# Kernel tuning notes

Measured on AMD Instinct MI355X. Metric: run time of the kernel, lower is better.

Reference implementation:

```python
import jax, jax.numpy as jnp
import numpy as np

N, E, DIN, DOUT, H = 50000, 800000, 256, 128, 8
DH = DOUT // H  # per-head dim = 16


def setup_inputs() -> dict:
    key = jax.random.key(0)
    k1, k2, k3, k4, k5 = jax.random.split(key, 5)
    x = jax.random.normal(k1, (N, DIN), dtype=jnp.float32)
    edge_index = jax.random.randint(k2, (2, E), 0, N)
    W_trans = jax.random.normal(k3, (DOUT, DIN), dtype=jnp.float32) / np.sqrt(DIN).astype(np.float32)
    W_att = jax.random.normal(k4, (1, 2 * DH), dtype=jnp.float32) / np.sqrt(2 * DH).astype(np.float32)
    b_att = jax.random.normal(k5, (1,), dtype=jnp.float32) * 0.01
    return {"x": x, "W_trans": W_trans, "W_att": W_att, "b_att": b_att, "edge_index": edge_index}


def reference(x, W_trans, W_att, b_att, edge_index):
    n = x.shape[0]
    # append self-loops (as in the torch module)
    loops = jnp.arange(n, dtype=edge_index.dtype)
    ei = jnp.concatenate([edge_index, jnp.stack([loops, loops])], axis=1)  # [2, E+N]
    src, dst = ei[0], ei[1]

    # linear transform, split heads: [n, H, DH]
    h = (x @ W_trans.T).reshape(n, H, DH)
    h_i = h[src]  # [Etot, H, DH]
    h_j = h[dst]  # [Etot, H, DH]

    # per-edge attention score: concat -> linear -> leaky_relu(0.2)
    s = jnp.concatenate([h_i, h_j], axis=-1) @ W_att.T + b_att  # [Etot, H, 1]
    s = jnp.where(s >= 0, s, 0.2 * s)

    # softmax(dim=0)*exp_sum/scatter_add(exp) == exp(s)/segment_sum(exp(s)) per dst node
    e = jnp.exp(s)
    denom = jax.ops.segment_sum(e, dst, num_segments=n)  # [n, H, 1]
    att = e / denom[dst]

    out = jax.ops.segment_sum(h_i * att, dst, num_segments=n)  # [n, H, DH]
    return out.reshape(n, DOUT)  # head_fusion='cat'
```

## Files before the change

### kernel.cpp

```cpp
#include <hip/hip_runtime.h>


constexpr int DIN  = 256;
constexpr int DOUT = 128;
constexpr int H    = 8;
constexpr int CAP  = 5120;
constexpr int NRANGE = 5;
constexpr int CHUNK = 4096;

typedef __attribute__((ext_vector_type(8))) short bf16x8;
typedef __attribute__((ext_vector_type(4))) float f32x4;

__device__ __forceinline__ float lrelu(float s) { return s >= 0.0f ? s : 0.2f * s; }

__device__ __forceinline__ unsigned short f2bf(float f) {
  unsigned u = __float_as_uint(f);
  u += 0x7FFF + ((u >> 16) & 1);
  return (unsigned short)(u >> 16);
}
__device__ __forceinline__ float bflo(unsigned u) { return __uint_as_float(u << 16); }
__device__ __forceinline__ float bfhi(unsigned u) { return __uint_as_float(u & 0xFFFF0000u); }
__device__ __forceinline__ int rng5(int s) {
  return (int)__umulhi((unsigned)s, 429497u);
}

__device__ __forceinline__ int wave_incl_scan(int v, int lane) {
#pragma unroll
  for (int d = 1; d < 64; d <<= 1) {
    int t = __shfl_up(v, d, 64);
    if (lane >= d) v += t;
  }
  return v;
}

__global__ void conv_w(const float* __restrict__ W, unsigned short* __restrict__ Wbf,
                       int n, int* __restrict__ bcount, int nb) {
  int i = blockIdx.x * blockDim.x + threadIdx.x;
  if (i < n) Wbf[i] = f2bf(W[i]);
  if (blockIdx.x == 0 && threadIdx.x < nb) bcount[threadIdx.x] = 0;
}

__global__ __launch_bounds__(256) void bp_gemm(const float* __restrict__ x,
                                               const unsigned short* __restrict__ Wbf,
                                               unsigned short* __restrict__ hbf, int N,
                                               const int* __restrict__ ei,
                                               int* __restrict__ bcount,
                                               unsigned* __restrict__ pair_buf,
                                               int E, int nb, int bp_blocks) {
  __shared__ int hist[256];
  __shared__ int gbase[256];
  if ((int)blockIdx.x < bp_blocks) {
    int c0 = blockIdx.x * CHUNK;
    hist[threadIdx.x] = 0;
    __syncthreads();
    int dcache[16];
#pragma unroll
    for (int q = 0; q < 16; ++q) {
      int e = c0 + q * 256 + threadIdx.x;
      dcache[q] = (e < E) ? ei[E + e] : -1;
      if (dcache[q] >= 0) atomicAdd(&hist[dcache[q] >> 8], 1);
    }
    __syncthreads();
    if (threadIdx.x < nb) {
      int c = hist[threadIdx.x];
      gbase[threadIdx.x] = c ? atomicAdd(&bcount[threadIdx.x], c) : 0;
    }
    __syncthreads();
    hist[threadIdx.x] = 0;
    __syncthreads();
#pragma unroll
    for (int q = 0; q < 16; ++q) {
      int e = c0 + q * 256 + threadIdx.x;
      if (dcache[q] >= 0) {
        int s = ei[e];
        int bk = dcache[q] >> 8;
        int r = atomicAdd(&hist[bk], 1);
        pair_buf[bk * CAP + gbase[bk] + r] = ((unsigned)s << 8) | (unsigned)(dcache[q] & 255);
      }
    }
    return;
  }
  int gb = blockIdx.x - bp_blocks;
  int tid = threadIdx.x;
  int w = tid >> 6, lane = tid & 63;
  int mr = lane & 15, kg = lane >> 4;
  int m0 = gb * 32 + (w >> 1) * 16;
  int nt0 = (w & 1) * 4;
  if (m0 >= N) return;
  int rr = m0 + mr;
  if (rr >= N) rr = N - 1;
  const float* xrow = x + (size_t)rr * DIN + kg * 8;

  float4 xa[8], xc[8];
#pragma unroll
  for (int ks = 0; ks < 8; ++ks) {
    xa[ks] = *(const float4*)(xrow + ks * 32);
    xc[ks] = *(const float4*)(xrow + ks * 32 + 4);
  }

  f32x4 acc[4];
#pragma unroll
  for (int t = 0; t < 4; ++t) acc[t] = (f32x4){0.f, 0.f, 0.f, 0.f};

#pragma unroll
  for (int ks = 0; ks < 8; ++ks) {
    bf16x8 a;
    a[0] = (short)f2bf(xa[ks].x); a[1] = (short)f2bf(xa[ks].y);
    a[2] = (short)f2bf(xa[ks].z); a[3] = (short)f2bf(xa[ks].w);
    a[4] = (short)f2bf(xc[ks].x); a[5] = (short)f2bf(xc[ks].y);
    a[6] = (short)f2bf(xc[ks].z); a[7] = (short)f2bf(xc[ks].w);
#pragma unroll
    for (int t = 0; t < 4; ++t) {
      bf16x8 b = *(const bf16x8*)(Wbf + ((nt0 + t) * 16 + mr) * DIN + ks * 32 + kg * 8);
      acc[t] = __builtin_amdgcn_mfma_f32_16x16x32_bf16(a, b, acc[t], 0, 0, 0);
    }
  }
#pragma unroll
  for (int t = 0; t < 4; ++t) {
#pragma unroll
    for (int r = 0; r < 4; ++r) {
      int row = m0 + kg * 4 + r;
      if (row < N) hbf[row * DOUT + (nt0 + t) * 16 + mr] = f2bf(acc[t][r]);
    }
  }
}

__global__ __launch_bounds__(256) void fs_ns(const unsigned* __restrict__ pair_buf,
                                             const int* __restrict__ bcount,
                                             int* __restrict__ offsets,
                                             uint4* __restrict__ len8,
                                             unsigned short* __restrict__ src_sorted,
                                             const unsigned short* __restrict__ hbf,
                                             const float* __restrict__ Wa,
                                             float* __restrict__ a_src,
                                             float* __restrict__ a_dst,
                                             int N, int E, int nb, int fs_blocks) {
  __shared__ int cnt[128 * NRANGE];
  __shared__ int cur[128 * NRANGE];
  __shared__ int redS[256];
  __shared__ int wsumS[4];
  __shared__ int lowerE;
  const int t = threadIdx.x;
  if ((int)blockIdx.x >= fs_blocks) {
    int idx = ((int)blockIdx.x - fs_blocks) * 256 + t;
    if (idx >= N * H) return;
    int v = idx >> 3, hh = idx & 7;
    const unsigned short* hp = hbf + (size_t)v * DOUT + hh * 16;
    uint4 p0 = *(const uint4*)hp;
    uint4 p1 = *(const uint4*)(hp + 8);
    float hv[16];
    hv[0] = bflo(p0.x); hv[1] = bfhi(p0.x); hv[2] = bflo(p0.y); hv[3] = bfhi(p0.y);
    hv[4] = bflo(p0.z); hv[5] = bfhi(p0.z); hv[6] = bflo(p0.w); hv[7] = bfhi(p0.w);
    hv[8] = bflo(p1.x); hv[9] = bfhi(p1.x); hv[10] = bflo(p1.y); hv[11] = bfhi(p1.y);
    hv[12] = bflo(p1.z); hv[13] = bfhi(p1.z); hv[14] = bflo(p1.w); hv[15] = bfhi(p1.w);
    float s1 = 0.f, s2 = 0.f;
#pragma unroll
    for (int d = 0; d < 16; ++d) {
      s1 += hv[d] * Wa[d];
      s2 += hv[d] * Wa[16 + d];
    }
    a_src[idx] = s1;
    a_dst[idx] = s2;
    return;
  }
  const int b = blockIdx.x;
  const int B = b >> 1, half = b & 1;
  const int node0 = b * 128;
  if (node0 >= N) return;
  for (int i = t; i < 128 * NRANGE; i += 256) cnt[i] = 0;
  if (t == 0) lowerE = 0;
  __syncthreads();
  const int v = node0 + t;
  int r_self = -1;
  if (t < 128 && v < N) {
    r_self = rng5(v);
    cnt[t * NRANGE + r_self] = 1;
  }
  __syncthreads();
  const int cntE = bcount[B];
  const unsigned* reg = pair_buf + B * CAP;
  for (int i = t; i < cntE; i += 256) {
    unsigned p = reg[i];
    int dl = p & 255;
    if ((dl >> 7) == half) atomicAdd(&cnt[(dl & 127) * NRANGE + rng5((int)(p >> 8))], 1);
    else if (half == 1) atomicAdd(&lowerE, 1);
  }
  redS[t] = (t < B) ? bcount[t] : 0;
  __syncthreads();
  for (int s = 128; s > 0; s >>= 1) {
    if (t < s) redS[t] += redS[t + s];
    __syncthreads();
  }
  int csr_base = redS[0] + B * 256 + (half ? (128 + lowerE) : 0);
  int tot = 0;
  if (t < 128) {
#pragma unroll
    for (int r = 0; r < NRANGE; ++r) tot += cnt[t * NRANGE + r];
  }
  int lane = t & 63, wv = t >> 6;
  int inc = wave_incl_scan(tot, lane);
  if (lane == 63) wsumS[wv] = inc;
  __syncthreads();
  int base = 0;
  for (int q = 0; q < wv; ++q) base += wsumS[q];
  int ex = base + inc - tot;
  if (t < 128 && v < N) {
    offsets[v] = csr_base + ex;
    int run = ex, rs_self = 0, c[NRANGE];
#pragma unroll
    for (int r = 0; r < NRANGE; ++r) {
      c[r] = cnt[t * NRANGE + r];
      if (r == r_self) rs_self = run;
      cur[t * NRANGE + r] = run + (r == r_self ? 1 : 0);
      run += c[r];
    }
    src_sorted[csr_base + rs_self] = (unsigned short)v;
    uint4 L;
    L.x = (unsigned)c[0] | ((unsigned)c[1] << 16);
    L.y = (unsigned)c[2] | ((unsigned)c[3] << 16);
    L.z = (unsigned)c[4];
    L.w = 0;
    len8[v] = L;
  }
  if (b == 0 && t == 0) offsets[N] = E + N;
  __syncthreads();
  for (int i = t; i < cntE; i += 256) {
    unsigned p = reg[i];
    int dl = p & 255;
    if ((dl >> 7) == half) {
      int s = (int)(p >> 8);
      int k = atomicAdd(&cur[(dl & 127) * NRANGE + rng5(s)], 1);
      src_sorted[csr_base + k] = (unsigned short)s;
    }
  }
}

__global__ __launch_bounds__(256) void aggregate(const unsigned short* __restrict__ hbf,
                                                 const float* __restrict__ a_src,
                                                 const float* __restrict__ a_dst,
                                                 const float* __restrict__ b_att,
                                                 const int* __restrict__ offsets,
                                                 const uint4* __restrict__ len8,
                                                 const unsigned short* __restrict__ src_sorted,
                                                 float* __restrict__ out, int N) {
  int wid = blockIdx.x * 4 + (threadIdx.x >> 6);
  if (wid >= N) return;
  int lane = threadIdx.x & 63;
  int g = lane >> 4, sl = lane & 15;
  int head = sl >> 1;
  float adv = a_dst[wid * H + head] + b_att[0];
  int j = offsets[wid];
  uint4 L = len8[wid];
  int lens[NRANGE];
  lens[0] = L.x & 0xffff; lens[1] = L.x >> 16;
  lens[2] = L.y & 0xffff; lens[3] = L.y >> 16;
  lens[4] = L.z;
  float a0 = 0, a1 = 0, a2 = 0, a3 = 0, a4 = 0, a5 = 0, a6 = 0, a7 = 0, den = 0;
  for (int r = 0; r < NRANGE; ++r) {
    int end = j + lens[r];
    for (int j0 = j; j0 < end; j0 += 4) {
      int jj = j0 + g;
      bool val = jj < end;
      int jc = val ? jj : end - 1;
      int s = src_sorted[jc];
      float as = a_src[s * H + head];
      uint4 u = *(const uint4*)(hbf + s * DOUT + sl * 8);
      float e = val ? __expf(lrelu(as + adv)) : 0.f;
      den += e;
      a0 += e * bflo(u.x); a1 += e * bfhi(u.x);
      a2 += e * bflo(u.y); a3 += e * bfhi(u.y);
      a4 += e * bflo(u.z); a5 += e * bfhi(u.z);
      a6 += e * bflo(u.w); a7 += e * bfhi(u.w);
    }
    j = end;
  }
  den += __shfl_xor(den, 16, 64); den += __shfl_xor(den, 32, 64);
  a0 += __shfl_xor(a0, 16, 64); a0 += __shfl_xor(a0, 32, 64);
  a1 += __shfl_xor(a1, 16, 64); a1 += __shfl_xor(a1, 32, 64);
  a2 += __shfl_xor(a2, 16, 64); a2 += __shfl_xor(a2, 32, 64);
  a3 += __shfl_xor(a3, 16, 64); a3 += __shfl_xor(a3, 32, 64);
  a4 += __shfl_xor(a4, 16, 64); a4 += __shfl_xor(a4, 32, 64);
  a5 += __shfl_xor(a5, 16, 64); a5 += __shfl_xor(a5, 32, 64);
  a6 += __shfl_xor(a6, 16, 64); a6 += __shfl_xor(a6, 32, 64);
  a7 += __shfl_xor(a7, 16, 64); a7 += __shfl_xor(a7, 32, 64);
  float inv = 1.0f / den;
  if (g == 0) {
    float4 o = make_float4(a0 * inv, a1 * inv, a2 * inv, a3 * inv);
    *(float4*)&out[wid * DOUT + sl * 8] = o;
  } else if (g == 1) {
    float4 o = make_float4(a4 * inv, a5 * inv, a6 * inv, a7 * inv);
    *(float4*)&out[wid * DOUT + sl * 8 + 4] = o;
  }
}

extern "C" void kernel_launch(void* const* d_in, const int* in_sizes, int n_in,
                              void* d_out, int out_size, void* d_ws, size_t ws_size,
                              hipStream_t stream) {
  const float* x     = (const float*)d_in[0];
  const float* W     = (const float*)d_in[1];
  const float* Wa    = (const float*)d_in[2];
  const float* b_att = (const float*)d_in[3];
  const int*   ei    = (const int*)d_in[4];
  const int N  = in_sizes[0] / DIN;
  const int E  = in_sizes[4] / 2;
  const int NB = (N + 255) / 256;
  float* out = (float*)d_out;

  char* p = (char*)d_ws;
  auto take = [&p](size_t bytes) {
    uintptr_t u = ((uintptr_t)p + 15) & ~(uintptr_t)15;
    p = (char*)(u + bytes);
    return (void*)u;
  };
  unsigned short* hbf = (unsigned short*)take((size_t)N * DOUT * 2);
  unsigned short* Wbf = (unsigned short*)take((size_t)DOUT * DIN * 2);
  float* a_src        = (float*)take((size_t)N * H * 4);
  float* a_dst        = (float*)take((size_t)N * H * 4);
  int* bcount         = (int*)take((size_t)NB * 4);
  unsigned* pair_buf  = (unsigned*)take((size_t)NB * CAP * 4);
  int* offsets        = (int*)take((size_t)(N + 1) * 4);
  uint4* len8         = (uint4*)take((size_t)N * 16);
  unsigned short* src_sorted = (unsigned short*)take((size_t)(E + N + 16) * 2);

  dim3 b256(256);
  const int bp_blocks   = (E + CHUNK - 1) / CHUNK;
  const int gemm_blocks = (N + 31) / 32;
  const int fs_blocks   = (N + 127) / 128;
  const int ns_blocks   = (N * H + 255) / 256;

  conv_w<<<dim3((DOUT * DIN + 255) / 256), b256, 0, stream>>>(W, Wbf, DOUT * DIN, bcount, NB);
  bp_gemm<<<dim3(bp_blocks + gemm_blocks), b256, 0, stream>>>(
      x, Wbf, hbf, N, ei, bcount, pair_buf, E, NB, bp_blocks);
  fs_ns<<<dim3(fs_blocks + ns_blocks), b256, 0, stream>>>(
      pair_buf, bcount, offsets, len8, src_sorted, hbf, Wa, a_src, a_dst, N, E, NB, fs_blocks);
  aggregate<<<dim3((N + 3) / 4), b256, 0, stream>>>(hbf, a_src, a_dst, b_att, offsets,
                                                    len8, src_sorted, out, N);
}
```

Measured before the change: 195.4 us.

## Drop source-range sub-bucketing in CSR build and shrink edge-binning chunk size

Removes the per-destination split of neighbors into five source-index ranges (and the len8 side array), so the CSR build uses one counter per node with 256-node blocks instead of two half-blocks. The aggregate kernel now loops over one contiguous neighbor range from offsets. The binning chunk shrinks from 4096 to 1024 edges per block, giving more blocks. The trade-off is simpler sorting and fewer loop boundaries in aggregation, but neighbors are no longer grouped by source range, which the old layout presumably used for gather cache locality.

```diff
diff --git a/kernel.cpp b/kernel.cpp
--- a/kernel.cpp
+++ b/kernel.cpp
@@ -5,8 +5,7 @@
 constexpr int DOUT = 128;
 constexpr int H    = 8;
 constexpr int CAP  = 5120;
-constexpr int NRANGE = 5;
-constexpr int CHUNK = 4096;
+constexpr int CHUNK = 1024;
 
 typedef __attribute__((ext_vector_type(8))) short bf16x8;
 typedef __attribute__((ext_vector_type(4))) float f32x4;
@@ -20,9 +19,6 @@
 }
 __device__ __forceinline__ float bflo(unsigned u) { return __uint_as_float(u << 16); }
 __device__ __forceinline__ float bfhi(unsigned u) { return __uint_as_float(u & 0xFFFF0000u); }
-__device__ __forceinline__ int rng5(int s) {
-  return (int)__umulhi((unsigned)s, 429497u);
-}
 
 __device__ __forceinline__ int wave_incl_scan(int v, int lane) {
 #pragma unroll
@@ -53,9 +49,9 @@
     int c0 = blockIdx.x * CHUNK;
     hist[threadIdx.x] = 0;
     __syncthreads();
-    int dcache[16];
-#pragma unroll
-    for (int q = 0; q < 16; ++q) {
+    int dcache[4];
+#pragma unroll
+    for (int q = 0; q < 4; ++q) {
       int e = c0 + q * 256 + threadIdx.x;
       dcache[q] = (e < E) ? ei[E + e] : -1;
       if (dcache[q] >= 0) atomicAdd(&hist[dcache[q] >> 8], 1);
@@ -69,7 +65,7 @@
     hist[threadIdx.x] = 0;
     __syncthreads();
 #pragma unroll
-    for (int q = 0; q < 16; ++q) {
+    for (int q = 0; q < 4; ++q) {
       int e = c0 + q * 256 + threadIdx.x;
       if (dcache[q] >= 0) {
         int s = ei[e];
@@ -128,21 +124,19 @@
 __global__ __launch_bounds__(256) void fs_ns(const unsigned* __restrict__ pair_buf,
                                              const int* __restrict__ bcount,
                                              int* __restrict__ offsets,
-                                             uint4* __restrict__ len8,
                                              unsigned short* __restrict__ src_sorted,
                                              const unsigned short* __restrict__ hbf,
                                              const float* __restrict__ Wa,
                                              float* __restrict__ a_src,
                                              float* __restrict__ a_dst,
-                                             int N, int E, int nb, int fs_blocks) {
-  __shared__ int cnt[128 * NRANGE];
-  __shared__ int cur[128 * NRANGE];
+                                             int N, int E, int nb) {
+  __shared__ int cnt[256];
+  __shared__ int cur[256];
   __shared__ int redS[256];
   __shared__ int wsumS[4];
-  __shared__ int lowerE;
   const int t = threadIdx.x;
-  if ((int)blockIdx.x >= fs_blocks) {
-    int idx = ((int)blockIdx.x - fs_blocks) * 256 + t;
+  if ((int)blockIdx.x >= nb) {
+    int idx = ((int)blockIdx.x - nb) * 256 + t;
     if (idx >= N * H) return;
     int v = idx >> 3, hh = idx & 7;
     const unsigned short* hp = hbf + (size_t)v * DOUT + hh * 16;
@@ -163,75 +157,42 @@
     a_dst[idx] = s2;
     return;
   }
-  const int b = blockIdx.x;
-  const int B = b >> 1, half = b & 1;
-  const int node0 = b * 128;
-  if (node0 >= N) return;
-  for (int i = t; i < 128 * NRANGE; i += 256) cnt[i] = 0;
-  if (t == 0) lowerE = 0;
-  __syncthreads();
+  const int B = blockIdx.x;
+  const int node0 = B * 256;
   const int v = node0 + t;
-  int r_self = -1;
-  if (t < 128 && v < N) {
-    r_self = rng5(v);
-    cnt[t * NRANGE + r_self] = 1;
-  }
+  const int valid = (v < N);
+  cnt[t] = valid ? 1 : 0;
   __syncthreads();
   const int cntE = bcount[B];
   const unsigned* reg = pair_buf + B * CAP;
+  for (int i = t; i < cntE; i += 256)
+    atomicAdd(&cnt[reg[i] & 255], 1);
+  redS[t] = (t < B) ? bcount[t] : 0;
+  __syncthreads();
+  for (int s = 128; s > 0; s >>= 1) {
+    if (t < s) redS[t] += redS[t + s];
+    __syncthreads();
+  }
+  const int csr_base = redS[0] + node0;
+  int val = cnt[t];
+  int lane = t & 63, wv = t >> 6;
+  int inc = wave_incl_scan(val, lane);
+  if (lane == 63) wsumS[wv] = inc;
+  __syncthreads();
+  int base = 0;
+  for (int q = 0; q < wv; ++q) base += wsumS[q];
+  int ex = base + inc - val;
+  cur[t] = ex + 1;
+  if (valid) {
+    offsets[v] = csr_base + ex;
+    src_sorted[csr_base + ex] = (unsigned short)v;
+  }
+  if (B == 0 && t == 0) offsets[N] = E + N;
+  __syncthreads();
   for (int i = t; i < cntE; i += 256) {
     unsigned p = reg[i];
-    int dl = p & 255;
-    if ((dl >> 7) == half) atomicAdd(&cnt[(dl & 127) * NRANGE + rng5((int)(p >> 8))], 1);
-    else if (half == 1) atomicAdd(&lowerE, 1);
-  }
-  redS[t] = (t < B) ? bcount[t] : 0;
-  __syncthreads();
-  for (int s = 128; s > 0; s >>= 1) {
-    if (t < s) redS[t] += redS[t + s];
-    __syncthreads();
-  }
-  int csr_base = redS[0] + B * 256 + (half ? (128 + lowerE) : 0);
-  int tot = 0;
-  if (t < 128) {
-#pragma unroll
-    for (int r = 0; r < NRANGE; ++r) tot += cnt[t * NRANGE + r];
-  }
-  int lane = t & 63, wv = t >> 6;
-  int inc = wave_incl_scan(tot, lane);
-  if (lane == 63) wsumS[wv] = inc;
-  __syncthreads();
-  int base = 0;
-  for (int q = 0; q < wv; ++q) base += wsumS[q];
-  int ex = base + inc - tot;
-  if (t < 128 && v < N) {
-    offsets[v] = csr_base + ex;
-    int run = ex, rs_self = 0, c[NRANGE];
-#pragma unroll
-    for (int r = 0; r < NRANGE; ++r) {
-      c[r] = cnt[t * NRANGE + r];
-      if (r == r_self) rs_self = run;
-      cur[t * NRANGE + r] = run + (r == r_self ? 1 : 0);
-      run += c[r];
-    }
-    src_sorted[csr_base + rs_self] = (unsigned short)v;
-    uint4 L;
-    L.x = (unsigned)c[0] | ((unsigned)c[1] << 16);
-    L.y = (unsigned)c[2] | ((unsigned)c[3] << 16);
-    L.z = (unsigned)c[4];
-    L.w = 0;
-    len8[v] = L;
-  }
-  if (b == 0 && t == 0) offsets[N] = E + N;
-  __syncthreads();
-  for (int i = t; i < cntE; i += 256) {
-    unsigned p = reg[i];
-    int dl = p & 255;
-    if ((dl >> 7) == half) {
-      int s = (int)(p >> 8);
-      int k = atomicAdd(&cur[(dl & 127) * NRANGE + rng5(s)], 1);
-      src_sorted[csr_base + k] = (unsigned short)s;
-    }
+    int k = atomicAdd(&cur[p & 255], 1);
+    src_sorted[csr_base + k] = (unsigned short)(p >> 8);
   }
 }
 
@@ -240,7 +201,6 @@
                                                  const float* __restrict__ a_dst,
                                                  const float* __restrict__ b_att,
                                                  const int* __restrict__ offsets,
-                                                 const uint4* __restrict__ len8,
                                                  const unsigned short* __restrict__ src_sorted,
                                                  float* __restrict__ out, int N) {
   int wid = blockIdx.x * 4 + (threadIdx.x >> 6);
@@ -249,30 +209,21 @@
   int g = lane >> 4, sl = lane & 15;
   int head = sl >> 1;
   float adv = a_dst[wid * H + head] + b_att[0];
-  int j = offsets[wid];
-  uint4 L = len8[wid];
-  int lens[NRANGE];
-  lens[0] = L.x & 0xffff; lens[1] = L.x >> 16;
-  lens[2] = L.y & 0xffff; lens[3] = L.y >> 16;
-  lens[4] = L.z;
+  int beg = offsets[wid], end = offsets[wid + 1];
   float a0 = 0, a1 = 0, a2 = 0, a3 = 0, a4 = 0, a5 = 0, a6 = 0, a7 = 0, den = 0;
-  for (int r = 0; r < NRANGE; ++r) {
-    int end = j + lens[r];
-    for (int j0 = j; j0 < end; j0 += 4) {
-      int jj = j0 + g;
-      bool val = jj < end;
-      int jc = val ? jj : end - 1;
-      int s = src_sorted[jc];
-      float as = a_src[s * H + head];
-      uint4 u = *(const uint4*)(hbf + s * DOUT + sl * 8);
-      float e = val ? __expf(lrelu(as + adv)) : 0.f;
-      den += e;
-      a0 += e * bflo(u.x); a1 += e * bfhi(u.x);
-      a2 += e * bflo(u.y); a3 += e * bfhi(u.y);
-      a4 += e * bflo(u.z); a5 += e * bfhi(u.z);
-      a6 += e * bflo(u.w); a7 += e * bfhi(u.w);
-    }
-    j = end;
+  for (int j0 = beg; j0 < end; j0 += 4) {
+    int jj = j0 + g;
+    bool valid = jj < end;
+    int jc = valid ? jj : beg;
+    int s = src_sorted[jc];
+    float as = a_src[s * H + head];
+    uint4 u = *(const uint4*)(hbf + s * DOUT + sl * 8);
+    float e = valid ? __expf(lrelu(as + adv)) : 0.f;
+    den += e;
+    a0 += e * bflo(u.x); a1 += e * bfhi(u.x);
+    a2 += e * bflo(u.y); a3 += e * bfhi(u.y);
+    a4 += e * bflo(u.z); a5 += e * bfhi(u.z);
+    a6 += e * bflo(u.w); a7 += e * bfhi(u.w);
   }
   den += __shfl_xor(den, 16, 64); den += __shfl_xor(den, 32, 64);
   a0 += __shfl_xor(a0, 16, 64); a0 += __shfl_xor(a0, 32, 64);
@@ -319,20 +270,18 @@
   int* bcount         = (int*)take((size_t)NB * 4);
   unsigned* pair_buf  = (unsigned*)take((size_t)NB * CAP * 4);
   int* offsets        = (int*)take((size_t)(N + 1) * 4);
-  uint4* len8         = (uint4*)take((size_t)N * 16);
   unsigned short* src_sorted = (unsigned short*)take((size_t)(E + N + 16) * 2);
 
   dim3 b256(256);
   const int bp_blocks   = (E + CHUNK - 1) / CHUNK;
   const int gemm_blocks = (N + 31) / 32;
-  const int fs_blocks   = (N + 127) / 128;
   const int ns_blocks   = (N * H + 255) / 256;
 
   conv_w<<<dim3((DOUT * DIN + 255) / 256), b256, 0, stream>>>(W, Wbf, DOUT * DIN, bcount, NB);
   bp_gemm<<<dim3(bp_blocks + gemm_blocks), b256, 0, stream>>>(
       x, Wbf, hbf, N, ei, bcount, pair_buf, E, NB, bp_blocks);
-  fs_ns<<<dim3(fs_blocks + ns_blocks), b256, 0, stream>>>(
-      pair_buf, bcount, offsets, len8, src_sorted, hbf, Wa, a_src, a_dst, N, E, NB, fs_blocks);
+  fs_ns<<<dim3(NB + ns_blocks), b256, 0, stream>>>(
+      pair_buf, bcount, offsets, src_sorted, hbf, Wa, a_src, a_dst, N, E, NB);
   aggregate<<<dim3((N + 3) / 4), b256, 0, stream>>>(hbf, a_src, a_dst, b_att, offsets,
-                                                    len8, src_sorted, out, N);
-}
+                                                    src_sorted, out, N);
+}
```

After: 202.5 us. 3.6% more time.
